# Kernel optimization log

Measured on AMD Instinct MI355X. Metric: run time of the kernel, lower is better.

## Reference

```python
import jax, jax.numpy as jnp
import numpy as np

KS = 3            # kernel_size per axis
K3 = KS * KS * KS  # 27 flattened kernel bins
_OFFSETS = np.array([[dz, dy, dx] for dz in (0, 1) for dy in (0, 1) for dx in (0, 1)], np.int32)  # 8 trilinear corners
_STRIDES = np.array([KS * KS, KS, 1], np.int32)
EPS = 1e-12


def continuous_conv(features, pos_input, pos_output, extents, kernel, bias):
    """Open3D-style ContinuousConv: ball_to_cube_radial mapping, poly6 window,
    trilinear kernel interpolation, per-output-point weighted aggregate."""
    No, Ni = pos_output.shape[0], pos_input.shape[0]
    # normalized relative positions: unit ball of radius extents/2 -> r in [0,1)
    rel = (pos_input[None, :, :] - pos_output[:, None, :]) * (2.0 / extents[0])  # [No,Ni,3]
    r2 = jnp.sum(rel * rel, axis=-1)                                             # [No,Ni]
    inside = r2 < 1.0
    window = jnp.where(inside, (1.0 - r2) ** 3, 0.0)        # poly6 window, zero outside support
    r = jnp.sqrt(jnp.maximum(r2, EPS))
    linf = jnp.max(jnp.abs(rel), axis=-1)
    # radial ball->cube map: scale each point by ||p||_2 / ||p||_inf
    scale = jnp.where(linf > EPS, r / jnp.maximum(linf, EPS), 1.0)
    q = jnp.clip(rel * scale[..., None], -1.0, 1.0)         # cube coords in [-1,1]^3
    t = (q + 1.0) * 0.5 * (KS - 1)                          # grid coords in [0, KS-1]
    t0 = jnp.clip(jnp.floor(t), 0, KS - 2).astype(jnp.int32)
    f = t - t0                                              # trilinear fractions [No,Ni,3]
    off = jnp.asarray(_OFFSETS)                             # [8,3]
    cw = jnp.where(off[None, None, :, :] == 1, f[:, :, None, :], 1.0 - f[:, :, None, :])
    w8 = cw.prod(axis=-1) * window[:, :, None]              # [No,Ni,8] corner weights
    idx8 = jnp.sum((t0[:, :, None, :] + off) * jnp.asarray(_STRIDES), axis=-1)  # [No,Ni,8] flat bin
    ii = jnp.arange(No)[:, None, None]
    jj = jnp.arange(Ni)[None, :, None]
    # A[i,j,k]: interpolation weight of input j into kernel bin k for output i
    A = jnp.zeros((No, Ni, K3), features.dtype).at[ii, jj, idx8].add(w8)
    B = jnp.einsum('ijk,jc->ikc', A, features)              # aggregate features per bin
    out = jnp.einsum('ikc,kcf->if', B, kernel) + bias       # contract with learned kernel
    return out


def setup_inputs() -> dict:
    key = jax.random.key(0)
    k1, k2, k3, k4 = jax.random.split(key, 4)
    N_IN, N_OUT, C_IN, C_OUT = 2048, 2048, 8, 64
    features = jax.random.normal(k1, (N_IN, C_IN), dtype=jnp.float32)
    pos_input = jax.random.uniform(k2, (N_IN, 3), dtype=jnp.float32)
    pos_output = jax.random.uniform(k3, (N_OUT, 3), dtype=jnp.float32)
    extents = jnp.ones((1,), dtype=jnp.float32)
    kernel = jax.random.normal(k4, (K3, C_IN, C_OUT), dtype=jnp.float32) * 0.05
    bias = jnp.zeros((C_OUT,), dtype=jnp.float32)
    return {"features": features, "pos_input": pos_input, "pos_output": pos_output,
            "extents": extents, "kernel": kernel, "bias": bias}


def reference(features, pos_input, pos_output, extents, kernel, bias):
    x = continuous_conv(features, pos_input, pos_output, extents, kernel, bias)
    return jax.nn.relu(x)
```

## Files before the change

### kernel.cpp

```cpp
#include <hip/hip_runtime.h>

#define K3 27
#define CIN 8
#define COUT 64
#define CC_EPS 1e-12f
#define CHUNK 32
#define RECW 12

__global__ __launch_bounds__(256, 8)
void cconv_fused_kernel(const float* __restrict__ features,
                        const float* __restrict__ pos_input,
                        const float* __restrict__ pos_output,
                        const float* __restrict__ extents,
                        const float* __restrict__ kern,
                        const float* __restrict__ bias,
                        float* __restrict__ out,
                        int Ni, int No)
{
    const int tid  = threadIdx.x;
    const int w    = tid >> 6;
    const int lane = tid & 63;
    const int g    = lane >> 3;
    const int c    = lane & 7;
    const int i    = blockIdx.x;

    __shared__ __align__(16) char smem[4096 + 4*CHUNK*RECW*4 + 4*K3*CIN*4];
    unsigned short* idx  = (unsigned short*)smem;
    float*          part = (float*)smem;
    float*          wrec = (float*)(smem + 4096);
    float*          Bsh  = (float*)(smem + 4096 + 4*CHUNK*RECW*4);
    __shared__ int cnt_sh;

    if (tid == 0) cnt_sh = 0;
    __syncthreads();

    const float s  = 2.0f / extents[0];
    const float ox = pos_output[i*3+0];
    const float oy = pos_output[i*3+1];
    const float oz = pos_output[i*3+2];

    for (int j0 = w*64; j0 < Ni; j0 += 256) {
        const int j = j0 + lane;
        bool inside = false;
        if (j < Ni) {
            const float rx = (pos_input[j*3+0]-ox)*s;
            const float ry = (pos_input[j*3+1]-oy)*s;
            const float rz = (pos_input[j*3+2]-oz)*s;
            inside = (rx*rx + ry*ry + rz*rz) < 1.0f;
        }
        const unsigned long long m = __ballot(inside);
        const int nin = (int)__popcll(m);
        int base = 0;
        if (lane == 0 && nin) base = atomicAdd(&cnt_sh, nin);
        base = __shfl(base, 0, 64);
        if (inside) {
            const int pre = __popcll(m & ((1ull<<lane)-1ull));
            idx[base+pre] = (unsigned short)j;
        }
    }
    __syncthreads();
    const int total = cnt_sh;

    float acc[K3];
#pragma unroll
    for (int k = 0; k < K3; ++k) acc[k] = 0.0f;

    for (int cb = w*CHUNK; cb < total; cb += 4*CHUNK) {
        if (lane < CHUNK) {
            const int  slot = cb + lane;
            const bool va   = slot < total;
            const int  j    = idx[va ? slot : 0];
            float ab0=0,ab1=0,ab2=0,ab3=0,ab4=0,ab5=0,ab6=0,ab7=0,ab8=0;
            float wc0=0,wc1=0,wc2=0;
            if (va) {
                const float rx = (pos_input[j*3+0]-ox)*s;
                const float ry = (pos_input[j*3+1]-oy)*s;
                const float rz = (pos_input[j*3+2]-oz)*s;
                const float r2  = rx*rx + ry*ry + rz*rz;
                const float u   = 1.0f - r2;
                const float win = u*u*u;
                const float r    = __builtin_amdgcn_sqrtf(fmaxf(r2, CC_EPS));
                const float linf = fmaxf(fmaxf(fabsf(rx), fabsf(ry)), fabsf(rz));
                const float scale = (linf > CC_EPS) ? r*__builtin_amdgcn_rcpf(linf) : 1.0f;
                const float ta = fminf(fmaxf(rx*scale, -1.f), 1.f) + 1.0f;
                const float tb = fminf(fmaxf(ry*scale, -1.f), 1.f) + 1.0f;
                const float tc = fminf(fmaxf(rz*scale, -1.f), 1.f) + 1.0f;
                const float wa0 = fmaxf(1.0f-ta, 0.0f), wa2 = fmaxf(ta-1.0f, 0.0f);
                const float wb0 = fmaxf(1.0f-tb, 0.0f), wb2 = fmaxf(tb-1.0f, 0.0f);
                wc0 = fmaxf(1.0f-tc, 0.0f); wc2 = fmaxf(tc-1.0f, 0.0f);
                const float wa1 = 1.0f - wa0 - wa2;
                const float wb1 = 1.0f - wb0 - wb2;
                wc1 = 1.0f - wc0 - wc2;
                const float a0 = wa0*win, a1 = wa1*win, a2 = wa2*win;
                ab0 = a0*wb0; ab1 = a0*wb1; ab2 = a0*wb2;
                ab3 = a1*wb0; ab4 = a1*wb1; ab5 = a1*wb2;
                ab6 = a2*wb0; ab7 = a2*wb1; ab8 = a2*wb2;
            }
            float* rec = wrec + (w*CHUNK + lane)*RECW;
            ((float4*)rec)[0] = make_float4(ab0, ab1, ab2, ab3);
            ((float4*)rec)[1] = make_float4(ab4, ab5, ab6, ab7);
            ((float4*)rec)[2] = make_float4(ab8, wc0, wc1, wc2);
        }
        asm volatile("s_waitcnt lgkmcnt(0)" ::: "memory");
        __builtin_amdgcn_sched_barrier(0);

#pragma unroll
        for (int t = 0; t < CHUNK/8; ++t) {
            const int l    = t*8 + g;
            const int slot = cb + l;
            const float* rec = wrec + (w*CHUNK + l)*RECW;
            const float4 r0 = ((const float4*)rec)[0];
            const float4 r1 = ((const float4*)rec)[1];
            const float4 r2 = ((const float4*)rec)[2];
            const int   jj = idx[slot < total ? slot : 0];
            const float fv = features[jj*CIN + c];
            const float wabv[9] = { r0.x, r0.y, r0.z, r0.w,
                                    r1.x, r1.y, r1.z, r1.w, r2.x };
            const float fcs[3]  = { r2.y*fv, r2.z*fv, r2.w*fv };
#pragma unroll
            for (int ab = 0; ab < 9; ++ab) {
#pragma unroll
                for (int cc = 0; cc < 3; ++cc) {
                    acc[ab*3 + cc] = fmaf(wabv[ab], fcs[cc], acc[ab*3 + cc]);
                }
            }
        }
    }

#pragma unroll
    for (int k = 0; k < K3; ++k) {
        float v = acc[k];
        v += __shfl_xor(v, 8, 64);
        v += __shfl_xor(v, 16, 64);
        v += __shfl_xor(v, 32, 64);
        acc[k] = v;
    }
    if (g == 0) {
#pragma unroll
        for (int k = 0; k < K3; ++k) Bsh[(w*K3 + k)*CIN + c] = acc[k];
    }
    __syncthreads();

    if (tid < K3*CIN) {
        const int k  = tid >> 3;
        const int cc = tid & 7;
        Bsh[k*CIN + cc] = Bsh[k*CIN + cc]
                        + Bsh[(K3   + k)*CIN + cc]
                        + Bsh[(2*K3 + k)*CIN + cc]
                        + Bsh[(3*K3 + k)*CIN + cc];
    }
    __syncthreads();

    {
        const int kb = w*7;
        const int ke = (kb + 7 < K3) ? kb + 7 : K3;
        float o = 0.0f;
        for (int k = kb; k < ke; ++k) {
#pragma unroll
            for (int cc = 0; cc < CIN; ++cc) {
                o = fmaf(Bsh[k*CIN + cc], kern[(k*CIN + cc)*COUT + lane], o);
            }
        }
        part[w*COUT + lane] = o;
    }
    __syncthreads();

    if (tid < COUT) {
        const float o = bias[tid] + part[tid] + part[COUT + tid]
                      + part[2*COUT + tid] + part[3*COUT + tid];
        out[i*COUT + tid] = fmaxf(o, 0.0f);
    }
}

extern "C" void kernel_launch(void* const* d_in, const int* in_sizes, int n_in,
                              void* d_out, int out_size, void* d_ws, size_t ws_size,
                              hipStream_t stream) {
    const float* features   = (const float*)d_in[0];
    const float* pos_input  = (const float*)d_in[1];
    const float* pos_output = (const float*)d_in[2];
    const float* extents    = (const float*)d_in[3];
    const float* kern       = (const float*)d_in[4];
    const float* bias       = (const float*)d_in[5];
    float* out = (float*)d_out;

    const int Ni = in_sizes[0] / CIN;
    const int No = in_sizes[2] / 3;

    dim3 block(256);
    dim3 grid(No);
    cconv_fused_kernel<<<grid, block, 0, stream>>>(features, pos_input, pos_output,
                                                   extents, kern, bias, out, Ni, No);
}
```

Measured before the change: 95.20 us.

## Use packed FP32 FMA with 2 channels per lane in aggregation loop

```diff
diff --git a/kernel.cpp b/kernel.cpp
--- a/kernel.cpp
+++ b/kernel.cpp
@@ -7,7 +7,17 @@
 #define CHUNK 32
 #define RECW 12
 
-__global__ __launch_bounds__(256, 8)
+typedef float v2f __attribute__((ext_vector_type(2)));
+
+static __device__ __forceinline__ v2f vfma2(v2f a, v2f b, v2f c) {
+#if __has_builtin(__builtin_elementwise_fma)
+    return __builtin_elementwise_fma(a, b, c);
+#else
+    return a * b + c;
+#endif
+}
+
+__global__ __launch_bounds__(256, 5)
 void cconv_fused_kernel(const float* __restrict__ features,
                         const float* __restrict__ pos_input,
                         const float* __restrict__ pos_output,
@@ -20,8 +30,8 @@
     const int tid  = threadIdx.x;
     const int w    = tid >> 6;
     const int lane = tid & 63;
-    const int g    = lane >> 3;
-    const int c    = lane & 7;
+    const int g4   = lane >> 2;
+    const int c2   = lane & 3;
     const int i    = blockIdx.x;
 
     __shared__ __align__(16) char smem[4096 + 4*CHUNK*RECW*4 + 4*K3*CIN*4];
@@ -61,11 +71,18 @@
     __syncthreads();
     const int total = cnt_sh;
 
-    float acc[K3];
-#pragma unroll
-    for (int k = 0; k < K3; ++k) acc[k] = 0.0f;
+    v2f acc[K3];
+#pragma unroll
+    for (int k = 0; k < K3; ++k) acc[k] = (v2f){0.0f, 0.0f};
 
     for (int cb = w*CHUNK; cb < total; cb += 4*CHUNK) {
+        const int sl0 = cb + g4;
+        const int sl1 = cb + 16 + g4;
+        const int jj0 = idx[(sl0 < total) ? sl0 : 0];
+        const int jj1 = idx[(sl1 < total) ? sl1 : 0];
+        const v2f fv0 = *(const v2f*)(features + jj0*CIN + 2*c2);
+        const v2f fv1 = *(const v2f*)(features + jj1*CIN + 2*c2);
+
         if (lane < CHUNK) {
             const int  slot = cb + lane;
             const bool va   = slot < total;
@@ -101,43 +118,52 @@
             ((float4*)rec)[1] = make_float4(ab4, ab5, ab6, ab7);
             ((float4*)rec)[2] = make_float4(ab8, wc0, wc1, wc2);
         }
-        asm volatile("s_waitcnt lgkmcnt(0)" ::: "memory");
-        __builtin_amdgcn_sched_barrier(0);
-
-#pragma unroll
-        for (int t = 0; t < CHUNK/8; ++t) {
-            const int l    = t*8 + g;
-            const int slot = cb + l;
-            const float* rec = wrec + (w*CHUNK + l)*RECW;
+
+        {
+            const float* rec = wrec + (w*CHUNK + g4)*RECW;
             const float4 r0 = ((const float4*)rec)[0];
             const float4 r1 = ((const float4*)rec)[1];
             const float4 r2 = ((const float4*)rec)[2];
-            const int   jj = idx[slot < total ? slot : 0];
-            const float fv = features[jj*CIN + c];
+            const v2f p0 = r2.y * fv0, p1 = r2.z * fv0, p2 = r2.w * fv0;
             const float wabv[9] = { r0.x, r0.y, r0.z, r0.w,
                                     r1.x, r1.y, r1.z, r1.w, r2.x };
-            const float fcs[3]  = { r2.y*fv, r2.z*fv, r2.w*fv };
 #pragma unroll
             for (int ab = 0; ab < 9; ++ab) {
-#pragma unroll
-                for (int cc = 0; cc < 3; ++cc) {
-                    acc[ab*3 + cc] = fmaf(wabv[ab], fcs[cc], acc[ab*3 + cc]);
-                }
+                const v2f wsp = { wabv[ab], wabv[ab] };
+                acc[ab*3+0] = vfma2(wsp, p0, acc[ab*3+0]);
+                acc[ab*3+1] = vfma2(wsp, p1, acc[ab*3+1]);
+                acc[ab*3+2] = vfma2(wsp, p2, acc[ab*3+2]);
+            }
+        }
+        {
+            const float* rec = wrec + (w*CHUNK + 16 + g4)*RECW;
+            const float4 r0 = ((const float4*)rec)[0];
+            const float4 r1 = ((const float4*)rec)[1];
+            const float4 r2 = ((const float4*)rec)[2];
+            const v2f p0 = r2.y * fv1, p1 = r2.z * fv1, p2 = r2.w * fv1;
+            const float wabv[9] = { r0.x, r0.y, r0.z, r0.w,
+                                    r1.x, r1.y, r1.z, r1.w, r2.x };
+#pragma unroll
+            for (int ab = 0; ab < 9; ++ab) {
+                const v2f wsp = { wabv[ab], wabv[ab] };
+                acc[ab*3+0] = vfma2(wsp, p0, acc[ab*3+0]);
+                acc[ab*3+1] = vfma2(wsp, p1, acc[ab*3+1]);
+                acc[ab*3+2] = vfma2(wsp, p2, acc[ab*3+2]);
             }
         }
     }
 
 #pragma unroll
     for (int k = 0; k < K3; ++k) {
-        float v = acc[k];
-        v += __shfl_xor(v, 8, 64);
-        v += __shfl_xor(v, 16, 64);
-        v += __shfl_xor(v, 32, 64);
-        acc[k] = v;
-    }
-    if (g == 0) {
-#pragma unroll
-        for (int k = 0; k < K3; ++k) Bsh[(w*K3 + k)*CIN + c] = acc[k];
+        float vx = acc[k].x, vy = acc[k].y;
+        vx += __shfl_xor(vx, 4, 64);  vy += __shfl_xor(vy, 4, 64);
+        vx += __shfl_xor(vx, 8, 64);  vy += __shfl_xor(vy, 8, 64);
+        vx += __shfl_xor(vx, 16, 64); vy += __shfl_xor(vy, 16, 64);
+        vx += __shfl_xor(vx, 32, 64); vy += __shfl_xor(vy, 32, 64);
+        if (g4 == 0) {
+            Bsh[(w*K3 + k)*CIN + 2*c2]     = vx;
+            Bsh[(w*K3 + k)*CIN + 2*c2 + 1] = vy;
+        }
     }
     __syncthreads();
 
```

Measured after the change: 103.4 us. 1.09x slower.

## Split input range across independent waves and move kernel contraction to second pass

Applied to the files above, without the earlier changes.

```diff
diff --git a/kernel.cpp b/kernel.cpp
--- a/kernel.cpp
+++ b/kernel.cpp
@@ -3,79 +3,75 @@
 #define K3 27
 #define CIN 8
 #define COUT 64
+#define K3C (K3*CIN)
 #define CC_EPS 1e-12f
 #define CHUNK 32
 #define RECW 12
+#define MAXS 8
 
 __global__ __launch_bounds__(256, 8)
-void cconv_fused_kernel(const float* __restrict__ features,
-                        const float* __restrict__ pos_input,
-                        const float* __restrict__ pos_output,
-                        const float* __restrict__ extents,
-                        const float* __restrict__ kern,
-                        const float* __restrict__ bias,
-                        float* __restrict__ out,
-                        int Ni, int No)
+void cconv_scatter_kernel(const float* __restrict__ features,
+                          const float* __restrict__ pos_input,
+                          const float* __restrict__ pos_output,
+                          const float* __restrict__ extents,
+                          float* __restrict__ Bpart,
+                          int Ni, int No, int S)
 {
     const int tid  = threadIdx.x;
     const int w    = tid >> 6;
     const int lane = tid & 63;
     const int g    = lane >> 3;
     const int c    = lane & 7;
-    const int i    = blockIdx.x;
-
-    __shared__ __align__(16) char smem[4096 + 4*CHUNK*RECW*4 + 4*K3*CIN*4];
-    unsigned short* idx  = (unsigned short*)smem;
-    float*          part = (float*)smem;
-    float*          wrec = (float*)(smem + 4096);
-    float*          Bsh  = (float*)(smem + 4096 + 4*CHUNK*RECW*4);
-    __shared__ int cnt_sh;
-
-    if (tid == 0) cnt_sh = 0;
-    __syncthreads();
-
-    const float s  = 2.0f / extents[0];
+    const int unit = blockIdx.x * 4 + w;
+
+    __shared__ unsigned short      idxs[4][512];
+    __shared__ __align__(16) float rec[4][CHUNK][RECW];
+
+    if (unit >= No * S) return;
+    const int i = unit / S;
+    const int s = unit - i * S;
+
+    const float sc = 2.0f / extents[0];
     const float ox = pos_output[i*3+0];
     const float oy = pos_output[i*3+1];
     const float oz = pos_output[i*3+2];
 
-    for (int j0 = w*64; j0 < Ni; j0 += 256) {
+    const int jb = (int)(((long long)Ni * s)       / S);
+    const int je = (int)(((long long)Ni * (s + 1)) / S);
+
+    int cnt = 0;
+    for (int j0 = jb; j0 < je; j0 += 64) {
         const int j = j0 + lane;
         bool inside = false;
-        if (j < Ni) {
-            const float rx = (pos_input[j*3+0]-ox)*s;
-            const float ry = (pos_input[j*3+1]-oy)*s;
-            const float rz = (pos_input[j*3+2]-oz)*s;
+        if (j < je) {
+            const float rx = (pos_input[j*3+0]-ox)*sc;
+            const float ry = (pos_input[j*3+1]-oy)*sc;
+            const float rz = (pos_input[j*3+2]-oz)*sc;
             inside = (rx*rx + ry*ry + rz*rz) < 1.0f;
         }
         const unsigned long long m = __ballot(inside);
-        const int nin = (int)__popcll(m);
-        int base = 0;
-        if (lane == 0 && nin) base = atomicAdd(&cnt_sh, nin);
-        base = __shfl(base, 0, 64);
         if (inside) {
             const int pre = __popcll(m & ((1ull<<lane)-1ull));
-            idx[base+pre] = (unsigned short)j;
-        }
-    }
-    __syncthreads();
-    const int total = cnt_sh;
+            idxs[w][cnt + pre] = (unsigned short)j;
+        }
+        cnt += (int)__popcll(m);
+    }
 
     float acc[K3];
 #pragma unroll
     for (int k = 0; k < K3; ++k) acc[k] = 0.0f;
 
-    for (int cb = w*CHUNK; cb < total; cb += 4*CHUNK) {
+    for (int cb = 0; cb < cnt; cb += CHUNK) {
         if (lane < CHUNK) {
             const int  slot = cb + lane;
-            const bool va   = slot < total;
-            const int  j    = idx[va ? slot : 0];
+            const bool va   = slot < cnt;
+            const int  j    = idxs[w][va ? slot : 0];
             float ab0=0,ab1=0,ab2=0,ab3=0,ab4=0,ab5=0,ab6=0,ab7=0,ab8=0;
             float wc0=0,wc1=0,wc2=0;
             if (va) {
-                const float rx = (pos_input[j*3+0]-ox)*s;
-                const float ry = (pos_input[j*3+1]-oy)*s;
-                const float rz = (pos_input[j*3+2]-oz)*s;
+                const float rx = (pos_input[j*3+0]-ox)*sc;
+                const float ry = (pos_input[j*3+1]-oy)*sc;
+                const float rz = (pos_input[j*3+2]-oz)*sc;
                 const float r2  = rx*rx + ry*ry + rz*rz;
                 const float u   = 1.0f - r2;
                 const float win = u*u*u;
@@ -96,10 +92,10 @@
                 ab3 = a1*wb0; ab4 = a1*wb1; ab5 = a1*wb2;
                 ab6 = a2*wb0; ab7 = a2*wb1; ab8 = a2*wb2;
             }
-            float* rec = wrec + (w*CHUNK + lane)*RECW;
-            ((float4*)rec)[0] = make_float4(ab0, ab1, ab2, ab3);
-            ((float4*)rec)[1] = make_float4(ab4, ab5, ab6, ab7);
-            ((float4*)rec)[2] = make_float4(ab8, wc0, wc1, wc2);
+            float* rp = &rec[w][lane][0];
+            ((float4*)rp)[0] = make_float4(ab0, ab1, ab2, ab3);
+            ((float4*)rp)[1] = make_float4(ab4, ab5, ab6, ab7);
+            ((float4*)rp)[2] = make_float4(ab8, wc0, wc1, wc2);
         }
         asm volatile("s_waitcnt lgkmcnt(0)" ::: "memory");
         __builtin_amdgcn_sched_barrier(0);
@@ -108,11 +104,11 @@
         for (int t = 0; t < CHUNK/8; ++t) {
             const int l    = t*8 + g;
             const int slot = cb + l;
-            const float* rec = wrec + (w*CHUNK + l)*RECW;
-            const float4 r0 = ((const float4*)rec)[0];
-            const float4 r1 = ((const float4*)rec)[1];
-            const float4 r2 = ((const float4*)rec)[2];
-            const int   jj = idx[slot < total ? slot : 0];
+            const float* rp = &rec[w][l][0];
+            const float4 r0 = ((const float4*)rp)[0];
+            const float4 r1 = ((const float4*)rp)[1];
+            const float4 r2 = ((const float4*)rp)[2];
+            const int   jj = idxs[w][slot < cnt ? slot : 0];
             const float fv = features[jj*CIN + c];
             const float wabv[9] = { r0.x, r0.y, r0.z, r0.w,
                                     r1.x, r1.y, r1.z, r1.w, r2.x };
@@ -120,8 +116,8 @@
 #pragma unroll
             for (int ab = 0; ab < 9; ++ab) {
 #pragma unroll
-                for (int cc = 0; cc < 3; ++cc) {
-                    acc[ab*3 + cc] = fmaf(wabv[ab], fcs[cc], acc[ab*3 + cc]);
+                for (int c3 = 0; c3 < 3; ++c3) {
+                    acc[ab*3 + c3] = fmaf(wabv[ab], fcs[c3], acc[ab*3 + c3]);
                 }
             }
         }
@@ -135,41 +131,45 @@
         v += __shfl_xor(v, 32, 64);
         acc[k] = v;
     }
-    if (g == 0) {
-#pragma unroll
-        for (int k = 0; k < K3; ++k) Bsh[(w*K3 + k)*CIN + c] = acc[k];
-    }
-    __syncthreads();
-
-    if (tid < K3*CIN) {
-        const int k  = tid >> 3;
-        const int cc = tid & 7;
-        Bsh[k*CIN + cc] = Bsh[k*CIN + cc]
-                        + Bsh[(K3   + k)*CIN + cc]
-                        + Bsh[(2*K3 + k)*CIN + cc]
-                        + Bsh[(3*K3 + k)*CIN + cc];
-    }
-    __syncthreads();
-
-    {
-        const int kb = w*7;
-        const int ke = (kb + 7 < K3) ? kb + 7 : K3;
-        float o = 0.0f;
-        for (int k = kb; k < ke; ++k) {
-#pragma unroll
-            for (int cc = 0; cc < CIN; ++cc) {
-                o = fmaf(Bsh[k*CIN + cc], kern[(k*CIN + cc)*COUT + lane], o);
-            }
-        }
-        part[w*COUT + lane] = o;
-    }
-    __syncthreads();
-
-    if (tid < COUT) {
-        const float o = bias[tid] + part[tid] + part[COUT + tid]
-                      + part[2*COUT + tid] + part[3*COUT + tid];
-        out[i*COUT + tid] = fmaxf(o, 0.0f);
-    }
+    if (lane < 8) {
+        float* dst = Bpart + (size_t)unit * K3C;
+#pragma unroll
+        for (int k = 0; k < K3; ++k) dst[k*CIN + lane] = acc[k];
+    }
+}
+
+__global__ __launch_bounds__(256)
+void cconv_gemm_kernel(const float* __restrict__ Bpart,
+                       const float* __restrict__ kern,
+                       const float* __restrict__ bias,
+                       float* __restrict__ out,
+                       int No, int S)
+{
+    const int tid = threadIdx.x;
+    const int w   = tid >> 6;
+    const int f   = tid & 63;
+    const int i   = blockIdx.x * 4 + w;
+
+    __shared__ float Bs[4][K3C];
+
+    if (i >= No) return;
+
+    for (int t = f; t < K3C; t += 64) {
+        const float* p = Bpart + (size_t)i * S * K3C + t;
+        float v = 0.0f;
+        for (int s = 0; s < S; ++s) v += p[s * K3C];
+        Bs[w][t] = v;
+    }
+
+    float o = bias[f];
+#pragma unroll 3
+    for (int k = 0; k < K3; ++k) {
+#pragma unroll
+        for (int cc = 0; cc < CIN; ++cc) {
+            o = fmaf(Bs[w][k*CIN + cc], kern[(k*CIN + cc)*COUT + f], o);
+        }
+    }
+    out[(size_t)i * COUT + f] = fmaxf(o, 0.0f);
 }
 
 extern "C" void kernel_launch(void* const* d_in, const int* in_sizes, int n_in,
@@ -186,8 +186,21 @@
     const int Ni = in_sizes[0] / CIN;
     const int No = in_sizes[2] / 3;
 
-    dim3 block(256);
-    dim3 grid(No);
-    cconv_fused_kernel<<<grid, block, 0, stream>>>(features, pos_input, pos_output,
-                                                   extents, kern, bias, out, Ni, No);
+    int S = MAXS;
+    while (S > 1 && (size_t)No * S * K3C * sizeof(float) > ws_size) S >>= 1;
+    float* Bpart = (float*)d_ws;
+
+    {
+        const int units = No * S;
+        dim3 block(256);
+        dim3 grid((units + 3) / 4);
+        cconv_scatter_kernel<<<grid, block, 0, stream>>>(features, pos_input,
+                                                         pos_output, extents,
+                                                         Bpart, Ni, No, S);
+    }
+    {
+        dim3 block(256);
+        dim3 grid((No + 3) / 4);
+        cconv_gemm_kernel<<<grid, block, 0, stream>>>(Bpart, kern, bias, out, No, S);
+    }
 }
```

Result: slower. 115.2 us (+21.0%).
